# Kernel tuning notes

Measured on AMD Instinct MI355X. Metric: run time of the kernel, lower is better.

## Reference

```python
import jax, jax.numpy as jnp
import numpy as np

NUM_FEATURES = 20480
NUM_ACC = 128
BATCH = 4096
SPARSITY_P = 0.0015  # ~30 active features per position, like real NNUE


def setup_inputs() -> dict:
    key = jax.random.key(0)
    kw, kb, k1, k2, k3, k4 = jax.random.split(key, 6)
    # sparse binary one-hot-per-piece feature vectors
    white = (jax.random.uniform(kw, (BATCH, NUM_FEATURES)) < SPARSITY_P).astype(jnp.float32)
    black = (jax.random.uniform(kb, (BATCH, NUM_FEATURES)) < SPARSITY_P).astype(jnp.float32)
    psqt_w = jax.random.normal(k1, (2, NUM_FEATURES), dtype=jnp.float32) * 0.02
    acc_w = jax.random.normal(k2, (NUM_ACC, NUM_FEATURES), dtype=jnp.float32) * 0.02
    acc_b = jax.random.normal(k3, (NUM_ACC,), dtype=jnp.float32) * 0.02
    out_w = jax.random.normal(k4, (2, NUM_ACC), dtype=jnp.float32) * 0.1
    return {"white": white, "black": black, "psqt_w": psqt_w,
            "acc_w": acc_w, "acc_b": acc_b, "out_w": out_w}


def _side(x, psqt_w, acc_w, acc_b, out_w):
    # psqt: [B,2]; accumulator: [B,128]; CReLU then Linear(128->2, no bias)
    psqt = x @ psqt_w.T                              # [B, 2]
    acc = jnp.clip(x @ acc_w.T + acc_b, 0.0, 1.0)    # [B, 128]
    pos = acc @ out_w.T                              # [B, 2]
    return psqt, pos


def reference(white, black, psqt_w, acc_w, acc_b, out_w):
    psqt_w_, pos_w = _side(white, psqt_w, acc_w, acc_b, out_w)
    psqt_b, pos_b = _side(black, psqt_w, acc_w, acc_b, out_w)
    return (psqt_w_ - psqt_b) + (pos_w - pos_b)      # [B, 2]
```

## Files before the change

kernel.cpp:

```cpp
#include <hip/hip_runtime.h>

#define NF   20480
#define NACC 128
#define BATCH 4096
#define MAXI 96
#define NSUB 8

typedef unsigned int uvec4 __attribute__((ext_vector_type(4)));
typedef float        fvec4 __attribute__((ext_vector_type(4)));

__global__ __launch_bounds__(256) void transpose_accw(const float* __restrict__ acc_w,
                                                      float* __restrict__ accT) {
    __shared__ float tile[NACC][33];
    const int t  = threadIdx.x;
    const int f0 = blockIdx.x * 32;
    const int fl = t & 31;
    const int cr = t >> 5;
    #pragma unroll
    for (int i = 0; i < 16; ++i) {
        int cc = i * 8 + cr;
        tile[cc][fl] = acc_w[(size_t)cc * NF + f0 + fl];
    }
    __syncthreads();
    const int c  = t & 127;
    const int fr = t >> 7;
    #pragma unroll
    for (int i = 0; i < 16; ++i) {
        int ff = i * 2 + fr;
        accT[(size_t)(f0 + ff) * NACC + c] = tile[c][ff];
    }
}

__global__ __launch_bounds__(256) void nnue_main(
    const float* __restrict__ white,
    const float* __restrict__ black,
    const float* __restrict__ psqt_w,
    const float* __restrict__ accT,
    const float* __restrict__ acc_b,
    const float* __restrict__ out_w,
    float* __restrict__ out)
{
    __shared__ int   s_cnt;
    __shared__ int   s_idx[MAXI];
    __shared__ fvec4 s_part[NSUB][32];
    __shared__ float s_red[4];
    __shared__ float s_ps[2];

    const int t = threadIdx.x;
    const int b = blockIdx.x;

    float bias = 0.f, ow0 = 0.f, ow1 = 0.f;
    if (t < NACC) { bias = acc_b[t]; ow0 = out_w[t]; ow1 = out_w[NACC + t]; }

    const int lane32 = t & 31;
    const int sub    = t >> 5;

    float res0 = 0.f, res1 = 0.f;

    for (int side = 0; side < 2; ++side) {
        const float* X = (side ? black : white) + (size_t)b * NF;
        const uvec4* Xv = (const uvec4*)X;

        if (t == 0) s_cnt = 0;
        __syncthreads();

        #pragma unroll
        for (int i = 0; i < 10; ++i) {
            int v = i * 512 + t;
            uvec4 a = __builtin_nontemporal_load(&Xv[v]);
            uvec4 c = __builtin_nontemporal_load(&Xv[v + 256]);
            if (a.x | a.y | a.z | a.w | c.x | c.y | c.z | c.w) {
                int ba = v * 4, bc = (v + 256) * 4;
                if (a.x) { int p = atomicAdd(&s_cnt, 1); if (p < MAXI) s_idx[p] = ba + 0; }
                if (a.y) { int p = atomicAdd(&s_cnt, 1); if (p < MAXI) s_idx[p] = ba + 1; }
                if (a.z) { int p = atomicAdd(&s_cnt, 1); if (p < MAXI) s_idx[p] = ba + 2; }
                if (a.w) { int p = atomicAdd(&s_cnt, 1); if (p < MAXI) s_idx[p] = ba + 3; }
                if (c.x) { int p = atomicAdd(&s_cnt, 1); if (p < MAXI) s_idx[p] = bc + 0; }
                if (c.y) { int p = atomicAdd(&s_cnt, 1); if (p < MAXI) s_idx[p] = bc + 1; }
                if (c.z) { int p = atomicAdd(&s_cnt, 1); if (p < MAXI) s_idx[p] = bc + 2; }
                if (c.w) { int p = atomicAdd(&s_cnt, 1); if (p < MAXI) s_idx[p] = bc + 3; }
            }
        }
        __syncthreads();
        const int n = min(s_cnt, MAXI);

        fvec4 acc4 = {0.f, 0.f, 0.f, 0.f};
        for (int j = sub; j < n; j += NSUB) {
            int f = s_idx[j];
            acc4 += *(const fvec4*)&accT[(size_t)f * NACC + lane32 * 4];
        }
        s_part[sub][lane32] = acc4;
        __syncthreads();

        float p0 = 0.f, p1 = 0.f;
        if (t < NACC) {
            const float* sp = (const float*)s_part;
            float a = 0.f;
            #pragma unroll
            for (int s2 = 0; s2 < NSUB; ++s2) a += sp[s2 * NACC + t];
            float h = fminf(fmaxf(a + bias, 0.f), 1.f);
            p0 = h * ow0;
            p1 = h * ow1;
            #pragma unroll
            for (int off = 32; off > 0; off >>= 1) {
                p0 += __shfl_down(p0, off, 64);
                p1 += __shfl_down(p1, off, 64);
            }
            if ((t & 63) == 0) { int wv = t >> 6; s_red[wv * 2] = p0; s_red[wv * 2 + 1] = p1; }
        } else {
            const int k  = t - NACC;
            const int ch = k >> 6;
            const int j0 = k & 63;
            float ps = 0.f;
            for (int j = j0; j < n; j += 64)
                ps += psqt_w[(size_t)ch * NF + s_idx[j]];
            #pragma unroll
            for (int off = 32; off > 0; off >>= 1)
                ps += __shfl_down(ps, off, 64);
            if (j0 == 0) s_ps[ch] = ps;
        }
        __syncthreads();

        if (t == 0) {
            float sgn = side ? -1.f : 1.f;
            res0 += sgn * (s_red[0] + s_red[2] + s_ps[0]);
            res1 += sgn * (s_red[1] + s_red[3] + s_ps[1]);
        }
    }

    if (t == 0) {
        out[(size_t)b * 2 + 0] = res0;
        out[(size_t)b * 2 + 1] = res1;
    }
}

extern "C" void kernel_launch(void* const* d_in, const int* in_sizes, int n_in,
                              void* d_out, int out_size, void* d_ws, size_t ws_size,
                              hipStream_t stream) {
    const float* white  = (const float*)d_in[0];
    const float* black  = (const float*)d_in[1];
    const float* psqt_w = (const float*)d_in[2];
    const float* acc_w  = (const float*)d_in[3];
    const float* acc_b  = (const float*)d_in[4];
    const float* out_w  = (const float*)d_in[5];
    float* out = (float*)d_out;

    float* accT = (float*)d_ws;

    transpose_accw<<<NF / 32, 256, 0, stream>>>(acc_w, accT);
    nnue_main<<<BATCH, 256, 0, stream>>>(white, black, psqt_w, accT,
                                         acc_b, out_w, out);
}
```

Measured before the change: 615.4 us.

## Process white and black sides concurrently in split thread halves

Each block now splits its 256 threads into two 128-thread halves, one per side, so the white and black scans, gathers and reductions run at the same time instead of one after the other. This removes the per-side loop and its barriers. The psqt lookup is folded into the scan: each thread accumulates psqt weights for the features it finds and adds them into the final wave reduction, removing a separate psqt gather pass. In exchange, each thread issues twice as many scan loads, and the accumulator gather uses 4 sub-groups per side instead of 8.

```diff
diff --git a/kernel.cpp b/kernel.cpp
--- a/kernel.cpp
+++ b/kernel.cpp
@@ -4,7 +4,6 @@
 #define NACC 128
 #define BATCH 4096
 #define MAXI 96
-#define NSUB 8
 
 typedef unsigned int uvec4 __attribute__((ext_vector_type(4)));
 typedef float        fvec4 __attribute__((ext_vector_type(4)));
@@ -31,6 +30,18 @@
     }
 }
 
+#define PROCV(u, base)                                                                               \
+    if (u.x | u.y | u.z | u.w) {                                                                     \
+        if (u.x) { int p = atomicAdd(cnt, 1); if (p < MAXI) idx[p] = (base) + 0;                     \
+                   ps0 += psqt_w[(base) + 0]; ps1 += psqt_w[NF + (base) + 0]; }                      \
+        if (u.y) { int p = atomicAdd(cnt, 1); if (p < MAXI) idx[p] = (base) + 1;                     \
+                   ps0 += psqt_w[(base) + 1]; ps1 += psqt_w[NF + (base) + 1]; }                      \
+        if (u.z) { int p = atomicAdd(cnt, 1); if (p < MAXI) idx[p] = (base) + 2;                     \
+                   ps0 += psqt_w[(base) + 2]; ps1 += psqt_w[NF + (base) + 2]; }                      \
+        if (u.w) { int p = atomicAdd(cnt, 1); if (p < MAXI) idx[p] = (base) + 3;                     \
+                   ps0 += psqt_w[(base) + 3]; ps1 += psqt_w[NF + (base) + 3]; }                      \
+    }
+
 __global__ __launch_bounds__(256) void nnue_main(
     const float* __restrict__ white,
     const float* __restrict__ black,
@@ -40,97 +51,79 @@
     const float* __restrict__ out_w,
     float* __restrict__ out)
 {
-    __shared__ int   s_cnt;
-    __shared__ int   s_idx[MAXI];
-    __shared__ fvec4 s_part[NSUB][32];
-    __shared__ float s_red[4];
-    __shared__ float s_ps[2];
+    __shared__ int   s_cnt[2];
+    __shared__ int   s_idx[2][MAXI];
+    __shared__ fvec4 s_part[2][4][32];
+    __shared__ float s_red[8];
 
-    const int t = threadIdx.x;
-    const int b = blockIdx.x;
+    const int t    = threadIdx.x;
+    const int b    = blockIdx.x;
+    const int side = t >> 7;
+    const int lt   = t & 127;
 
-    float bias = 0.f, ow0 = 0.f, ow1 = 0.f;
-    if (t < NACC) { bias = acc_b[t]; ow0 = out_w[t]; ow1 = out_w[NACC + t]; }
+    const float bias = acc_b[lt];
+    const float ow0  = out_w[lt];
+    const float ow1  = out_w[NACC + lt];
+    const float sgn  = side ? -1.f : 1.f;
 
-    const int lane32 = t & 31;
-    const int sub    = t >> 5;
+    const float* X  = (side ? black : white) + (size_t)b * NF;
+    const uvec4* Xv = (const uvec4*)X;
 
-    float res0 = 0.f, res1 = 0.f;
+    if (t < 2) s_cnt[t] = 0;
+    __syncthreads();
 
-    for (int side = 0; side < 2; ++side) {
-        const float* X = (side ? black : white) + (size_t)b * NF;
-        const uvec4* Xv = (const uvec4*)X;
+    float ps0 = 0.f, ps1 = 0.f;
+    int* cnt = &s_cnt[side];
+    int* idx = s_idx[side];
 
-        if (t == 0) s_cnt = 0;
-        __syncthreads();
-
-        #pragma unroll
-        for (int i = 0; i < 10; ++i) {
-            int v = i * 512 + t;
-            uvec4 a = __builtin_nontemporal_load(&Xv[v]);
-            uvec4 c = __builtin_nontemporal_load(&Xv[v + 256]);
-            if (a.x | a.y | a.z | a.w | c.x | c.y | c.z | c.w) {
-                int ba = v * 4, bc = (v + 256) * 4;
-                if (a.x) { int p = atomicAdd(&s_cnt, 1); if (p < MAXI) s_idx[p] = ba + 0; }
-                if (a.y) { int p = atomicAdd(&s_cnt, 1); if (p < MAXI) s_idx[p] = ba + 1; }
-                if (a.z) { int p = atomicAdd(&s_cnt, 1); if (p < MAXI) s_idx[p] = ba + 2; }
-                if (a.w) { int p = atomicAdd(&s_cnt, 1); if (p < MAXI) s_idx[p] = ba + 3; }
-                if (c.x) { int p = atomicAdd(&s_cnt, 1); if (p < MAXI) s_idx[p] = bc + 0; }
-                if (c.y) { int p = atomicAdd(&s_cnt, 1); if (p < MAXI) s_idx[p] = bc + 1; }
-                if (c.z) { int p = atomicAdd(&s_cnt, 1); if (p < MAXI) s_idx[p] = bc + 2; }
-                if (c.w) { int p = atomicAdd(&s_cnt, 1); if (p < MAXI) s_idx[p] = bc + 3; }
-            }
-        }
-        __syncthreads();
-        const int n = min(s_cnt, MAXI);
-
-        fvec4 acc4 = {0.f, 0.f, 0.f, 0.f};
-        for (int j = sub; j < n; j += NSUB) {
-            int f = s_idx[j];
-            acc4 += *(const fvec4*)&accT[(size_t)f * NACC + lane32 * 4];
-        }
-        s_part[sub][lane32] = acc4;
-        __syncthreads();
-
-        float p0 = 0.f, p1 = 0.f;
-        if (t < NACC) {
-            const float* sp = (const float*)s_part;
-            float a = 0.f;
-            #pragma unroll
-            for (int s2 = 0; s2 < NSUB; ++s2) a += sp[s2 * NACC + t];
-            float h = fminf(fmaxf(a + bias, 0.f), 1.f);
-            p0 = h * ow0;
-            p1 = h * ow1;
-            #pragma unroll
-            for (int off = 32; off > 0; off >>= 1) {
-                p0 += __shfl_down(p0, off, 64);
-                p1 += __shfl_down(p1, off, 64);
-            }
-            if ((t & 63) == 0) { int wv = t >> 6; s_red[wv * 2] = p0; s_red[wv * 2 + 1] = p1; }
-        } else {
-            const int k  = t - NACC;
-            const int ch = k >> 6;
-            const int j0 = k & 63;
-            float ps = 0.f;
-            for (int j = j0; j < n; j += 64)
-                ps += psqt_w[(size_t)ch * NF + s_idx[j]];
-            #pragma unroll
-            for (int off = 32; off > 0; off >>= 1)
-                ps += __shfl_down(ps, off, 64);
-            if (j0 == 0) s_ps[ch] = ps;
-        }
-        __syncthreads();
-
-        if (t == 0) {
-            float sgn = side ? -1.f : 1.f;
-            res0 += sgn * (s_red[0] + s_red[2] + s_ps[0]);
-            res1 += sgn * (s_red[1] + s_red[3] + s_ps[1]);
+    #pragma unroll 2
+    for (int i = 0; i < 10; ++i) {
+        const int v = i * 512 + lt;
+        uvec4 a0 = __builtin_nontemporal_load(&Xv[v]);
+        uvec4 a1 = __builtin_nontemporal_load(&Xv[v + 128]);
+        uvec4 a2 = __builtin_nontemporal_load(&Xv[v + 256]);
+        uvec4 a3 = __builtin_nontemporal_load(&Xv[v + 384]);
+        if (a0.x|a0.y|a0.z|a0.w | a1.x|a1.y|a1.z|a1.w |
+            a2.x|a2.y|a2.z|a2.w | a3.x|a3.y|a3.z|a3.w) {
+            PROCV(a0, (v      ) * 4)
+            PROCV(a1, (v + 128) * 4)
+            PROCV(a2, (v + 256) * 4)
+            PROCV(a3, (v + 384) * 4)
         }
     }
+    __syncthreads();
+
+    const int n      = min(s_cnt[side], MAXI);
+    const int sub    = (t >> 5) & 3;
+    const int lane32 = t & 31;
+    const int* sIdx  = s_idx[side];
+
+    fvec4 acc4 = {0.f, 0.f, 0.f, 0.f};
+    for (int j = sub; j < n; j += 4) {
+        int f = sIdx[j];
+        acc4 += *(const fvec4*)&accT[(size_t)f * NACC + lane32 * 4];
+    }
+    s_part[side][sub][lane32] = acc4;
+    __syncthreads();
+
+    const float* sp = (const float*)&s_part[side][0][0];
+    float a = sp[0 * NACC + lt] + sp[1 * NACC + lt]
+            + sp[2 * NACC + lt] + sp[3 * NACC + lt];
+    float h  = fminf(fmaxf(a + bias, 0.f), 1.f);
+    float p0 = sgn * (h * ow0 + ps0);
+    float p1 = sgn * (h * ow1 + ps1);
+
+    #pragma unroll
+    for (int off = 32; off > 0; off >>= 1) {
+        p0 += __shfl_down(p0, off, 64);
+        p1 += __shfl_down(p1, off, 64);
+    }
+    if ((t & 63) == 0) { int wv = t >> 6; s_red[wv * 2] = p0; s_red[wv * 2 + 1] = p1; }
+    __syncthreads();
 
     if (t == 0) {
-        out[(size_t)b * 2 + 0] = res0;
-        out[(size_t)b * 2 + 1] = res1;
+        out[(size_t)b * 2 + 0] = s_red[0] + s_red[2] + s_red[4] + s_red[6];
+        out[(size_t)b * 2 + 1] = s_red[1] + s_red[3] + s_red[5] + s_red[7];
     }
 }
 
```

Measured after the change: 606.9 us. No clear change (-1.4%).
